# Kernel tuning notes

Measured on AMD Instinct MI355X. Metric: run time of the kernel, lower is better.

The kernel has to match this reference:

```python
import jax, jax.numpy as jnp
import numpy as np

N_EMBD = 1024
HEAD_SIZE = 64
WINDOW_SIZE = 256


def setup_inputs() -> dict:
    key = jax.random.key(0)
    kx, kk, kq, kv = jax.random.split(key, 4)
    B, T = 4, 4096
    x = jax.random.normal(kx, (B, T, N_EMBD), dtype=jnp.float32)
    # Linear(n_embd, head_size, bias=False): y = x @ W where W is [n_embd, head_size]
    scale = 1.0 / np.sqrt(N_EMBD)
    Wk = jax.random.normal(kk, (N_EMBD, HEAD_SIZE), dtype=jnp.float32) * scale
    Wq = jax.random.normal(kq, (N_EMBD, HEAD_SIZE), dtype=jnp.float32) * scale
    Wv = jax.random.normal(kv, (N_EMBD, HEAD_SIZE), dtype=jnp.float32) * scale
    return {"x": x, "Wk": Wk, "Wq": Wq, "Wv": Wv}


def reference(x, Wk, Wq, Wv):
    B, T, C = x.shape
    k = jnp.einsum('btc,ch->bth', x, Wk)  # [B,T,H]
    q = jnp.einsum('btc,ch->bth', x, Wq)
    v = jnp.einsum('btc,ch->bth', x, Wv)
    scale = k.shape[-1] ** -0.5
    weights = jnp.einsum('bqh,bkh->bqk', q, k) * scale  # [B,T,T]
    rows = jnp.arange(T)[:, None]
    cols = jnp.arange(T)[None, :]
    # causal AND within sliding window of WINDOW_SIZE
    mask = (rows >= cols) & (cols >= rows - WINDOW_SIZE + 1)
    weights = jnp.where(mask, weights, -jnp.inf)
    weights = jax.nn.softmax(weights, axis=-1)
    out = jnp.einsum('bqk,bkh->bqh', weights, v)  # [B,T,H]
    return out
```

## Files before the change

kernel.cpp:

```cpp
#include <hip/hip_runtime.h>
#include <float.h>

#define TSEQ 4096
#define CEMB 1024
#define NH 64
#define WIN 256

typedef __attribute__((ext_vector_type(8))) short  s16x8;
typedef __attribute__((ext_vector_type(4))) short  s16x4;
typedef __attribute__((ext_vector_type(4))) float  f32x4;

__device__ __forceinline__ void split2(float f, short& hi, short& lo) {
    unsigned b = __float_as_uint(f);
    hi = (short)(b >> 16);
    float hf = __uint_as_float(b & 0xFFFF0000u);
    lo = (short)(__float_as_uint(f - hf) >> 16);
}

__device__ __forceinline__ void split8(f32x4 a, f32x4 b, s16x8& hi, s16x8& lo) {
    #pragma unroll
    for (int j = 0; j < 4; ++j) { short h, l; split2(a[j], h, l); hi[j] = h; lo[j] = l; }
    #pragma unroll
    for (int j = 0; j < 4; ++j) { short h, l; split2(b[j], h, l); hi[4+j] = h; lo[4+j] = l; }
}

#define MFMA(a, b, c) __builtin_amdgcn_mfma_f32_16x16x32_bf16((a), (b), (c), 0, 0, 0)

__global__ __launch_bounds__(256)
void w_convert(const float* __restrict__ Wk, const float* __restrict__ Wq,
               const float* __restrict__ Wv,
               short* __restrict__ Wth, short* __restrict__ Wtl)
{
    const int m  = blockIdx.x >> 4;
    const int k0 = (blockIdx.x & 15) << 6;
    const float* src = (m == 0) ? Wk : ((m == 1) ? Wq : Wv);
    #pragma unroll
    for (int i = 0; i < 16; ++i) {
        const int idx = threadIdx.x + (i << 8);
        const int r = idx >> 6, c = idx & 63;
        const float v = src[(k0 + r) * NH + c];
        short h, l; split2(v, h, l);
        const int o = (m * 64 + c) * CEMB + k0 + r;
        Wth[o] = h; Wtl[o] = l;
    }
}

__device__ __forceinline__ int swz(int row, int chunk) {
    return row * 32 + (((chunk) ^ ((row >> 1) & 3)) << 3);
}

__global__ __launch_bounds__(256)
void qkv_proj(const float* __restrict__ x,
              const short* __restrict__ Wth, const short* __restrict__ Wtl,
              float* __restrict__ kb, float* __restrict__ qb, float* __restrict__ vb)
{
    __shared__ short Ah[2][64 * 32], Al[2][64 * 32];
    __shared__ short Bh[2][192 * 32], Bl[2][192 * 32];

    const int tid = threadIdx.x;
    const int m0  = blockIdx.x << 6;
    const int w   = tid >> 6;
    const int l15 = tid & 15;
    const int g   = (tid >> 4) & 3;

    const int arow = tid >> 2;
    const int ach  = tid & 3;
    const float* xp = x + (size_t)(m0 + arow) * CEMB + (ach << 3);

    int wn[3], wch[3];
    #pragma unroll
    for (int i = 0; i < 3; ++i) {
        const int c = tid + (i << 8);
        wn[i] = c >> 2; wch[i] = c & 3;
    }

    f32x4 acc[4][3];
    #pragma unroll
    for (int i = 0; i < 4; ++i)
        #pragma unroll
        for (int j = 0; j < 3; ++j) acc[i][j] = (f32x4){0.f, 0.f, 0.f, 0.f};

    f32x4 xr0 = *(const f32x4*)(xp);
    f32x4 xr1 = *(const f32x4*)(xp + 4);
    s16x8 wrh[3], wrl[3];
    #pragma unroll
    for (int i = 0; i < 3; ++i) {
        const int o = wn[i] * CEMB + (wch[i] << 3);
        wrh[i] = *(const s16x8*)&Wth[o];
        wrl[i] = *(const s16x8*)&Wtl[o];
    }

    for (int t = 0; t < 32; ++t) {
        const int cur = t & 1;
        {
            s16x8 vh, vl; split8(xr0, xr1, vh, vl);
            const int ao = swz(arow, ach);
            *(s16x8*)&Ah[cur][ao] = vh;
            *(s16x8*)&Al[cur][ao] = vl;
            #pragma unroll
            for (int i = 0; i < 3; ++i) {
                const int bo = swz(wn[i], wch[i]);
                *(s16x8*)&Bh[cur][bo] = wrh[i];
                *(s16x8*)&Bl[cur][bo] = wrl[i];
            }
        }
        __syncthreads();
        if (t < 31) {
            const int k0 = (t + 1) << 5;
            xr0 = *(const f32x4*)(xp + k0);
            xr1 = *(const f32x4*)(xp + k0 + 4);
            #pragma unroll
            for (int i = 0; i < 3; ++i) {
                const int o = wn[i] * CEMB + k0 + (wch[i] << 3);
                wrh[i] = *(const s16x8*)&Wth[o];
                wrl[i] = *(const s16x8*)&Wtl[o];
            }
        }
        s16x8 afh[4], afl[4], bfh[3], bfl[3];
        #pragma unroll
        for (int rt = 0; rt < 4; ++rt) {
            const int o = swz(rt * 16 + l15, g);
            afh[rt] = *(const s16x8*)&Ah[cur][o];
            afl[rt] = *(const s16x8*)&Al[cur][o];
        }
        #pragma unroll
        for (int ct = 0; ct < 3; ++ct) {
            const int n = w * 48 + ct * 16 + l15;
            const int o = swz(n, g);
            bfh[ct] = *(const s16x8*)&Bh[cur][o];
            bfl[ct] = *(const s16x8*)&Bl[cur][o];
        }
        #pragma unroll
        for (int rt = 0; rt < 4; ++rt)
            #pragma unroll
            for (int ct = 0; ct < 3; ++ct) {
                acc[rt][ct] = MFMA(afh[rt], bfh[ct], acc[rt][ct]);
                acc[rt][ct] = MFMA(afh[rt], bfl[ct], acc[rt][ct]);
                acc[rt][ct] = MFMA(afl[rt], bfh[ct], acc[rt][ct]);
            }
    }

    #pragma unroll
    for (int ct = 0; ct < 3; ++ct) {
        const int colbase = w * 48 + ct * 16;
        float* op = (colbase < 64) ? kb : ((colbase < 128) ? qb : vb);
        const int col = (colbase & 63) + l15;
        #pragma unroll
        for (int rt = 0; rt < 4; ++rt)
            #pragma unroll
            for (int r = 0; r < 4; ++r) {
                const int row = m0 + rt * 16 + g * 4 + r;
                op[(size_t)row * NH + col] = acc[rt][ct][r];
            }
    }
}

__global__ __launch_bounds__(256)
void attn_swin(const float* __restrict__ qb, const float* __restrict__ kb,
               const float* __restrict__ vb, float* __restrict__ out)
{
    __shared__ short Kh[64 * 72], Kl[64 * 72];
    __shared__ short Vth[64 * 72], Vtl[64 * 72];
    __shared__ short Ph[4][16 * 72], Pl[4][16 * 72];

    const int tid = threadIdx.x;
    const int Q0  = blockIdx.x << 6;
    const size_t base = (size_t)blockIdx.y * TSEQ;
    const int w   = tid >> 6;
    const int l15 = tid & 15;
    const int g   = (tid >> 4) & 3;

    const int qrow = Q0 + w * 16 + l15;

    s16x8 Qh[2], Ql[2];
    #pragma unroll
    for (int ks = 0; ks < 2; ++ks) {
        const float* qp = qb + (base + qrow) * NH + ks * 32 + g * 8;
        f32x4 a = *(const f32x4*)qp;
        f32x4 b = *(const f32x4*)(qp + 4);
        split8(a, b, Qh[ks], Ql[ks]);
    }

    f32x4 O[4];
    #pragma unroll
    for (int i = 0; i < 4; ++i) O[i] = (f32x4){0.f, 0.f, 0.f, 0.f};
    float m_run = -FLT_MAX, l_run = 0.f;

    int lo = Q0 - (WIN - 1); if (lo < 0) lo = 0;
    const int t_lo = lo >> 6, t_hi = Q0 >> 6;

    for (int t = t_lo; t <= t_hi; ++t) {
        const int k0 = t << 6;
        __syncthreads();
        #pragma unroll
        for (int i = 0; i < 4; ++i) {
            const int idx = tid + (i << 8);
            const int key = idx >> 4, c4 = (idx & 15) << 2;
            f32x4 kv = *(const f32x4*)&kb[(base + k0 + key) * NH + c4];
            s16x4 h, l;
            #pragma unroll
            for (int j = 0; j < 4; ++j) { short hh, ll; split2(kv[j], hh, ll); h[j] = hh; l[j] = ll; }
            *(s16x4*)&Kh[key * 72 + c4] = h;
            *(s16x4*)&Kl[key * 72 + c4] = l;
        }
        #pragma unroll
        for (int i = 0; i < 2; ++i) {
            const int item = tid + (i << 8);
            const int dim = item & 63, kb8 = (item >> 6) << 3;
            f32x4 v0, v1;
            #pragma unroll
            for (int kk = 0; kk < 4; ++kk)
                v0[kk] = vb[(base + k0 + kb8 + kk) * NH + dim];
            #pragma unroll
            for (int kk = 0; kk < 4; ++kk)
                v1[kk] = vb[(base + k0 + kb8 + 4 + kk) * NH + dim];
            s16x8 h, l; split8(v0, v1, h, l);
            *(s16x8*)&Vth[dim * 72 + kb8] = h;
            *(s16x8*)&Vtl[dim * 72 + kb8] = l;
        }
        __syncthreads();

        f32x4 S[4];
        #pragma unroll
        for (int kt = 0; kt < 4; ++kt) {
            f32x4 s = (f32x4){0.f, 0.f, 0.f, 0.f};
            #pragma unroll
            for (int ks = 0; ks < 2; ++ks) {
                const int o = (kt * 16 + l15) * 72 + ks * 32 + g * 8;
                s16x8 kah = *(const s16x8*)&Kh[o];
                s16x8 kal = *(const s16x8*)&Kl[o];
                s = MFMA(kah, Qh[ks], s);
                s = MFMA(kah, Ql[ks], s);
                s = MFMA(kal, Qh[ks], s);
            }
            S[kt] = s;
        }

        float sv[16]; bool vd[16];
        float mt = -FLT_MAX;
        #pragma unroll
        for (int kt = 0; kt < 4; ++kt)
            #pragma unroll
            for (int r = 0; r < 4; ++r) {
                const int key = k0 + kt * 16 + g * 4 + r;
                const float s = S[kt][r] * 0.125f;
                const bool v = (key <= qrow) && (key > qrow - WIN);
                sv[kt * 4 + r] = s; vd[kt * 4 + r] = v;
                if (v) mt = fmaxf(mt, s);
            }
        mt = fmaxf(mt, __shfl_xor(mt, 16));
        mt = fmaxf(mt, __shfl_xor(mt, 32));
        const float mn  = fmaxf(m_run, mt);
        const float fsc = __expf(m_run - mn);
        float sum = 0.f;
        #pragma unroll
        for (int kt = 0; kt < 4; ++kt)
            #pragma unroll
            for (int r = 0; r < 4; ++r) {
                const float p = vd[kt * 4 + r] ? __expf(sv[kt * 4 + r] - mn) : 0.f;
                sum += p;
                short h, l; split2(p, h, l);
                const int pc = kt * 16 + g * 4 + r;
                Ph[w][l15 * 72 + pc] = h;
                Pl[w][l15 * 72 + pc] = l;
            }
        sum += __shfl_xor(sum, 16);
        sum += __shfl_xor(sum, 32);
        l_run = l_run * fsc + sum;
        m_run = mn;

        float fr[4];
        #pragma unroll
        for (int r = 0; r < 4; ++r) fr[r] = __shfl(fsc, g * 4 + r);
        #pragma unroll
        for (int dt = 0; dt < 4; ++dt)
            #pragma unroll
            for (int r = 0; r < 4; ++r) O[dt][r] *= fr[r];

        #pragma unroll
        for (int ks = 0; ks < 2; ++ks) {
            const int po = l15 * 72 + ks * 32 + g * 8;
            s16x8 pah = *(const s16x8*)&Ph[w][po];
            s16x8 pal = *(const s16x8*)&Pl[w][po];
            #pragma unroll
            for (int dt = 0; dt < 4; ++dt) {
                const int vo = (dt * 16 + l15) * 72 + ks * 32 + g * 8;
                s16x8 vbh = *(const s16x8*)&Vth[vo];
                s16x8 vbl = *(const s16x8*)&Vtl[vo];
                O[dt] = MFMA(pah, vbh, O[dt]);
                O[dt] = MFMA(pah, vbl, O[dt]);
                O[dt] = MFMA(pal, vbh, O[dt]);
            }
        }
    }

    const float linv = 1.f / l_run;
    float fr[4];
    #pragma unroll
    for (int r = 0; r < 4; ++r) fr[r] = __shfl(linv, g * 4 + r);
    #pragma unroll
    for (int dt = 0; dt < 4; ++dt)
        #pragma unroll
        for (int r = 0; r < 4; ++r) {
            const int row = Q0 + w * 16 + g * 4 + r;
            out[(base + row) * NH + dt * 16 + l15] = O[dt][r] * fr[r];
        }
}

extern "C" void kernel_launch(void* const* d_in, const int* in_sizes, int n_in,
                              void* d_out, int out_size, void* d_ws, size_t ws_size,
                              hipStream_t stream)
{
    const float* x  = (const float*)d_in[0];
    const float* Wk = (const float*)d_in[1];
    const float* Wq = (const float*)d_in[2];
    const float* Wv = (const float*)d_in[3];
    float* out = (float*)d_out;

    const int Bn = in_sizes[0] / (TSEQ * CEMB);
    const size_t perBuf = (size_t)Bn * TSEQ * NH;

    float* kb = (float*)d_ws;
    float* qb = kb + perBuf;
    float* vb = qb + perBuf;
    short* Wth = (short*)(vb + perBuf);
    short* Wtl = Wth + 192 * CEMB;

    w_convert<<<dim3(48), dim3(256), 0, stream>>>(Wk, Wq, Wv, Wth, Wtl);
    qkv_proj<<<dim3((Bn * TSEQ) / 64), dim3(256), 0, stream>>>(x, Wth, Wtl, kb, qb, vb);
    attn_swin<<<dim3(TSEQ / 64, Bn), dim3(256), 0, stream>>>(qb, kb, vb, out);
}
```

Before: 153.5 us.

## Store QKV as bf16 hi/lo pairs, pre-transpose V, split-K attention across warps

The projection kernel now writes Q/K/V already split into bf16 high/low halves and uses 32-row tiles to launch twice as many blocks. A new kernel pre-transposes V so the attention kernel can read K and V fragments straight from global memory without staging them in shared memory or synchronising per tile. Attention now gives each block 16 query rows and spreads the key tiles across its four warps, then merges the partial softmax states through shared memory. This aims to remove the repeated fp32-to-bf16 conversion and the per-tile barriers, and to raise parallelism. In exchange it adds an extra kernel launch and more workspace traffic, and K/V are now read uncached from global memory by several blocks that share the same keys.

```diff
diff --git a/kernel.cpp b/kernel.cpp
--- a/kernel.cpp
+++ b/kernel.cpp
@@ -7,21 +7,21 @@
 #define WIN 256
 
 typedef __attribute__((ext_vector_type(8))) short  s16x8;
-typedef __attribute__((ext_vector_type(4))) short  s16x4;
 typedef __attribute__((ext_vector_type(4))) float  f32x4;
-
-__device__ __forceinline__ void split2(float f, short& hi, short& lo) {
+typedef unsigned short ush;
+
+__device__ __forceinline__ void split2(float f, ush& hi, ush& lo) {
     unsigned b = __float_as_uint(f);
-    hi = (short)(b >> 16);
+    hi = (ush)(b >> 16);
     float hf = __uint_as_float(b & 0xFFFF0000u);
-    lo = (short)(__float_as_uint(f - hf) >> 16);
+    lo = (ush)(__float_as_uint(f - hf) >> 16);
 }
 
 __device__ __forceinline__ void split8(f32x4 a, f32x4 b, s16x8& hi, s16x8& lo) {
     #pragma unroll
-    for (int j = 0; j < 4; ++j) { short h, l; split2(a[j], h, l); hi[j] = h; lo[j] = l; }
-    #pragma unroll
-    for (int j = 0; j < 4; ++j) { short h, l; split2(b[j], h, l); hi[4+j] = h; lo[4+j] = l; }
+    for (int j = 0; j < 4; ++j) { ush h, l; split2(a[j], h, l); hi[j] = (short)h; lo[j] = (short)l; }
+    #pragma unroll
+    for (int j = 0; j < 4; ++j) { ush h, l; split2(b[j], h, l); hi[4+j] = (short)h; lo[4+j] = (short)l; }
 }
 
 #define MFMA(a, b, c) __builtin_amdgcn_mfma_f32_16x16x32_bf16((a), (b), (c), 0, 0, 0)
@@ -29,7 +29,7 @@
 __global__ __launch_bounds__(256)
 void w_convert(const float* __restrict__ Wk, const float* __restrict__ Wq,
                const float* __restrict__ Wv,
-               short* __restrict__ Wth, short* __restrict__ Wtl)
+               ush* __restrict__ Wth, ush* __restrict__ Wtl)
 {
     const int m  = blockIdx.x >> 4;
     const int k0 = (blockIdx.x & 15) << 6;
@@ -39,7 +39,7 @@
         const int idx = threadIdx.x + (i << 8);
         const int r = idx >> 6, c = idx & 63;
         const float v = src[(k0 + r) * NH + c];
-        short h, l; split2(v, h, l);
+        ush h, l; split2(v, h, l);
         const int o = (m * 64 + c) * CEMB + k0 + r;
         Wth[o] = h; Wtl[o] = l;
     }
@@ -51,21 +51,24 @@
 
 __global__ __launch_bounds__(256)
 void qkv_proj(const float* __restrict__ x,
-              const short* __restrict__ Wth, const short* __restrict__ Wtl,
-              float* __restrict__ kb, float* __restrict__ qb, float* __restrict__ vb)
-{
-    __shared__ short Ah[2][64 * 32], Al[2][64 * 32];
+              const ush* __restrict__ Wth, const ush* __restrict__ Wtl,
+              ush* __restrict__ kbh, ush* __restrict__ kbl,
+              ush* __restrict__ qbh, ush* __restrict__ qbl,
+              ush* __restrict__ vbh, ush* __restrict__ vbl)
+{
+    __shared__ short Ah[2][32 * 32], Al[2][32 * 32];
     __shared__ short Bh[2][192 * 32], Bl[2][192 * 32];
 
     const int tid = threadIdx.x;
-    const int m0  = blockIdx.x << 6;
+    const int m0  = blockIdx.x << 5;
     const int w   = tid >> 6;
     const int l15 = tid & 15;
     const int g   = (tid >> 4) & 3;
 
-    const int arow = tid >> 2;
-    const int ach  = tid & 3;
-    const float* xp = x + (size_t)(m0 + arow) * CEMB + (ach << 3);
+    const bool aact = tid < 128;
+    const int arow  = tid >> 2;
+    const int ach   = tid & 3;
+    const float* xp = x + (size_t)(m0 + (aact ? arow : 0)) * CEMB + (ach << 3);
 
     int wn[3], wch[3];
     #pragma unroll
@@ -74,14 +77,14 @@
         wn[i] = c >> 2; wch[i] = c & 3;
     }
 
-    f32x4 acc[4][3];
-    #pragma unroll
-    for (int i = 0; i < 4; ++i)
+    f32x4 acc[2][3];
+    #pragma unroll
+    for (int i = 0; i < 2; ++i)
         #pragma unroll
         for (int j = 0; j < 3; ++j) acc[i][j] = (f32x4){0.f, 0.f, 0.f, 0.f};
 
-    f32x4 xr0 = *(const f32x4*)(xp);
-    f32x4 xr1 = *(const f32x4*)(xp + 4);
+    f32x4 xr0 = {0,0,0,0}, xr1 = {0,0,0,0};
+    if (aact) { xr0 = *(const f32x4*)(xp); xr1 = *(const f32x4*)(xp + 4); }
     s16x8 wrh[3], wrl[3];
     #pragma unroll
     for (int i = 0; i < 3; ++i) {
@@ -92,23 +95,22 @@
 
     for (int t = 0; t < 32; ++t) {
         const int cur = t & 1;
-        {
+        if (aact) {
             s16x8 vh, vl; split8(xr0, xr1, vh, vl);
             const int ao = swz(arow, ach);
             *(s16x8*)&Ah[cur][ao] = vh;
             *(s16x8*)&Al[cur][ao] = vl;
-            #pragma unroll
-            for (int i = 0; i < 3; ++i) {
-                const int bo = swz(wn[i], wch[i]);
-                *(s16x8*)&Bh[cur][bo] = wrh[i];
-                *(s16x8*)&Bl[cur][bo] = wrl[i];
-            }
+        }
+        #pragma unroll
+        for (int i = 0; i < 3; ++i) {
+            const int bo = swz(wn[i], wch[i]);
+            *(s16x8*)&Bh[cur][bo] = wrh[i];
+            *(s16x8*)&Bl[cur][bo] = wrl[i];
         }
         __syncthreads();
         if (t < 31) {
             const int k0 = (t + 1) << 5;
-            xr0 = *(const f32x4*)(xp + k0);
-            xr1 = *(const f32x4*)(xp + k0 + 4);
+            if (aact) { xr0 = *(const f32x4*)(xp + k0); xr1 = *(const f32x4*)(xp + k0 + 4); }
             #pragma unroll
             for (int i = 0; i < 3; ++i) {
                 const int o = wn[i] * CEMB + k0 + (wch[i] << 3);
@@ -116,22 +118,21 @@
                 wrl[i] = *(const s16x8*)&Wtl[o];
             }
         }
-        s16x8 afh[4], afl[4], bfh[3], bfl[3];
-        #pragma unroll
-        for (int rt = 0; rt < 4; ++rt) {
+        s16x8 afh[2], afl[2], bfh[3], bfl[3];
+        #pragma unroll
+        for (int rt = 0; rt < 2; ++rt) {
             const int o = swz(rt * 16 + l15, g);
             afh[rt] = *(const s16x8*)&Ah[cur][o];
             afl[rt] = *(const s16x8*)&Al[cur][o];
         }
         #pragma unroll
         for (int ct = 0; ct < 3; ++ct) {
-            const int n = w * 48 + ct * 16 + l15;
-            const int o = swz(n, g);
+            const int o = swz(w * 48 + ct * 16 + l15, g);
             bfh[ct] = *(const s16x8*)&Bh[cur][o];
             bfl[ct] = *(const s16x8*)&Bl[cur][o];
         }
         #pragma unroll
-        for (int rt = 0; rt < 4; ++rt)
+        for (int rt = 0; rt < 2; ++rt)
             #pragma unroll
             for (int ct = 0; ct < 3; ++ct) {
                 acc[rt][ct] = MFMA(afh[rt], bfh[ct], acc[rt][ct]);
@@ -143,42 +144,78 @@
     #pragma unroll
     for (int ct = 0; ct < 3; ++ct) {
         const int colbase = w * 48 + ct * 16;
-        float* op = (colbase < 64) ? kb : ((colbase < 128) ? qb : vb);
+        ush* oph; ush* opl;
+        if (colbase < 64)       { oph = kbh; opl = kbl; }
+        else if (colbase < 128) { oph = qbh; opl = qbl; }
+        else                    { oph = vbh; opl = vbl; }
         const int col = (colbase & 63) + l15;
         #pragma unroll
-        for (int rt = 0; rt < 4; ++rt)
+        for (int rt = 0; rt < 2; ++rt)
             #pragma unroll
             for (int r = 0; r < 4; ++r) {
-                const int row = m0 + rt * 16 + g * 4 + r;
-                op[(size_t)row * NH + col] = acc[rt][ct][r];
+                const size_t row = m0 + rt * 16 + g * 4 + r;
+                ush h, l; split2(acc[rt][ct][r], h, l);
+                oph[row * NH + col] = h;
+                opl[row * NH + col] = l;
             }
     }
 }
 
 __global__ __launch_bounds__(256)
-void attn_swin(const float* __restrict__ qb, const float* __restrict__ kb,
-               const float* __restrict__ vb, float* __restrict__ out)
-{
-    __shared__ short Kh[64 * 72], Kl[64 * 72];
-    __shared__ short Vth[64 * 72], Vtl[64 * 72];
-    __shared__ short Ph[4][16 * 72], Pl[4][16 * 72];
+void v_transpose(const ush* __restrict__ vbh, const ush* __restrict__ vbl,
+                 ush* __restrict__ vbTh, ush* __restrict__ vbTl)
+{
+    const int k0  = blockIdx.x << 6;
+    const int b   = blockIdx.y;
+    const int dim = threadIdx.x & 63;
+    const int j16 = threadIdx.x >> 6;
+    const size_t inb = ((size_t)b * TSEQ + k0 + j16 * 16) * NH + dim;
+    s16x8 h0, h1, l0, l1;
+    #pragma unroll
+    for (int j = 0; j < 8; ++j) {
+        h0[j] = (short)vbh[inb + (size_t)j * NH];
+        l0[j] = (short)vbl[inb + (size_t)j * NH];
+    }
+    #pragma unroll
+    for (int j = 0; j < 8; ++j) {
+        h1[j] = (short)vbh[inb + (size_t)(8 + j) * NH];
+        l1[j] = (short)vbl[inb + (size_t)(8 + j) * NH];
+    }
+    const size_t ob = (size_t)b * (64 * TSEQ) + (size_t)dim * TSEQ + k0 + j16 * 16;
+    *(s16x8*)&vbTh[ob]     = h0;
+    *(s16x8*)&vbTh[ob + 8] = h1;
+    *(s16x8*)&vbTl[ob]     = l0;
+    *(s16x8*)&vbTl[ob + 8] = l1;
+}
+
+__global__ __launch_bounds__(256)
+void attn_swin(const ush* __restrict__ qbh, const ush* __restrict__ qbl,
+               const ush* __restrict__ kbh, const ush* __restrict__ kbl,
+               const ush* __restrict__ vbTh, const ush* __restrict__ vbTl,
+               float* __restrict__ out)
+{
+    __shared__ ush Ph[4][16 * 64], Pl[4][16 * 64];
+    __shared__ float cO[4][16][68];
+    __shared__ float cm[4][16], cl[4][16];
 
     const int tid = threadIdx.x;
-    const int Q0  = blockIdx.x << 6;
-    const size_t base = (size_t)blockIdx.y * TSEQ;
     const int w   = tid >> 6;
     const int l15 = tid & 15;
     const int g   = (tid >> 4) & 3;
-
-    const int qrow = Q0 + w * 16 + l15;
+    const int u   = l15 & 7;
+    const int q0  = blockIdx.x << 4;
+    const int b   = blockIdx.y;
+    const size_t tbase = (size_t)b * TSEQ;
+    const size_t vtb   = (size_t)b * (64 * TSEQ);
+
+    const int qrow = q0 + l15;
 
     s16x8 Qh[2], Ql[2];
     #pragma unroll
     for (int ks = 0; ks < 2; ++ks) {
-        const float* qp = qb + (base + qrow) * NH + ks * 32 + g * 8;
-        f32x4 a = *(const f32x4*)qp;
-        f32x4 b = *(const f32x4*)(qp + 4);
-        split8(a, b, Qh[ks], Ql[ks]);
+        const size_t o = (tbase + qrow) * NH + ks * 32 + g * 8;
+        Qh[ks] = *(const s16x8*)&qbh[o];
+        Ql[ks] = *(const s16x8*)&qbl[o];
     }
 
     f32x4 O[4];
@@ -186,39 +223,11 @@
     for (int i = 0; i < 4; ++i) O[i] = (f32x4){0.f, 0.f, 0.f, 0.f};
     float m_run = -FLT_MAX, l_run = 0.f;
 
-    int lo = Q0 - (WIN - 1); if (lo < 0) lo = 0;
-    const int t_lo = lo >> 6, t_hi = Q0 >> 6;
-
-    for (int t = t_lo; t <= t_hi; ++t) {
+    int lo = q0 - (WIN - 1); if (lo < 0) lo = 0;
+    const int t_lo = lo >> 6, t_hi = q0 >> 6;
+
+    for (int t = t_lo + w; t <= t_hi; t += 4) {
         const int k0 = t << 6;
-        __syncthreads();
-        #pragma unroll
-        for (int i = 0; i < 4; ++i) {
-            const int idx = tid + (i << 8);
-            const int key = idx >> 4, c4 = (idx & 15) << 2;
-            f32x4 kv = *(const f32x4*)&kb[(base + k0 + key) * NH + c4];
-            s16x4 h, l;
-            #pragma unroll
-            for (int j = 0; j < 4; ++j) { short hh, ll; split2(kv[j], hh, ll); h[j] = hh; l[j] = ll; }
-            *(s16x4*)&Kh[key * 72 + c4] = h;
-            *(s16x4*)&Kl[key * 72 + c4] = l;
-        }
-        #pragma unroll
-        for (int i = 0; i < 2; ++i) {
-            const int item = tid + (i << 8);
-            const int dim = item & 63, kb8 = (item >> 6) << 3;
-            f32x4 v0, v1;
-            #pragma unroll
-            for (int kk = 0; kk < 4; ++kk)
-                v0[kk] = vb[(base + k0 + kb8 + kk) * NH + dim];
-            #pragma unroll
-            for (int kk = 0; kk < 4; ++kk)
-                v1[kk] = vb[(base + k0 + kb8 + 4 + kk) * NH + dim];
-            s16x8 h, l; split8(v0, v1, h, l);
-            *(s16x8*)&Vth[dim * 72 + kb8] = h;
-            *(s16x8*)&Vtl[dim * 72 + kb8] = l;
-        }
-        __syncthreads();
 
         f32x4 S[4];
         #pragma unroll
@@ -226,17 +235,16 @@
             f32x4 s = (f32x4){0.f, 0.f, 0.f, 0.f};
             #pragma unroll
             for (int ks = 0; ks < 2; ++ks) {
-                const int o = (kt * 16 + l15) * 72 + ks * 32 + g * 8;
-                s16x8 kah = *(const s16x8*)&Kh[o];
-                s16x8 kal = *(const s16x8*)&Kl[o];
-                s = MFMA(kah, Qh[ks], s);
-                s = MFMA(kah, Ql[ks], s);
-                s = MFMA(kal, Qh[ks], s);
+                const size_t o = (tbase + k0 + kt * 16 + l15) * NH + ks * 32 + g * 8;
+                s16x8 kh = *(const s16x8*)&kbh[o];
+                s16x8 kl = *(const s16x8*)&kbl[o];
+                s = MFMA(kh, Qh[ks], s);
+                s = MFMA(kh, Ql[ks], s);
+                s = MFMA(kl, Qh[ks], s);
             }
             S[kt] = s;
         }
 
-        float sv[16]; bool vd[16];
         float mt = -FLT_MAX;
         #pragma unroll
         for (int kt = 0; kt < 4; ++kt)
@@ -244,26 +252,34 @@
             for (int r = 0; r < 4; ++r) {
                 const int key = k0 + kt * 16 + g * 4 + r;
                 const float s = S[kt][r] * 0.125f;
-                const bool v = (key <= qrow) && (key > qrow - WIN);
-                sv[kt * 4 + r] = s; vd[kt * 4 + r] = v;
-                if (v) mt = fmaxf(mt, s);
+                S[kt][r] = s;
+                if ((key <= qrow) && (key > qrow - WIN)) mt = fmaxf(mt, s);
             }
         mt = fmaxf(mt, __shfl_xor(mt, 16));
         mt = fmaxf(mt, __shfl_xor(mt, 32));
         const float mn  = fmaxf(m_run, mt);
         const float fsc = __expf(m_run - mn);
+
         float sum = 0.f;
         #pragma unroll
-        for (int kt = 0; kt < 4; ++kt)
-            #pragma unroll
-            for (int r = 0; r < 4; ++r) {
-                const float p = vd[kt * 4 + r] ? __expf(sv[kt * 4 + r] - mn) : 0.f;
-                sum += p;
-                short h, l; split2(p, h, l);
-                const int pc = kt * 16 + g * 4 + r;
-                Ph[w][l15 * 72 + pc] = h;
-                Pl[w][l15 * 72 + pc] = l;
-            }
+        for (int kt = 0; kt < 4; ++kt) {
+            const int chunk = kt * 2 + (g >> 1);
+            const int c2 = (chunk + u) & 7;
+            const int abase = l15 * 64 + c2 * 8 + (g & 1) * 4;
+            #pragma unroll
+            for (int rp = 0; rp < 4; rp += 2) {
+                const int key0 = k0 + kt * 16 + g * 4 + rp;
+                const bool v0 = (key0     <= qrow) && (key0     > qrow - WIN);
+                const bool v1 = (key0 + 1 <= qrow) && (key0 + 1 > qrow - WIN);
+                const float p0 = v0 ? __expf(S[kt][rp]     - mn) : 0.f;
+                const float p1 = v1 ? __expf(S[kt][rp + 1] - mn) : 0.f;
+                sum += p0 + p1;
+                ush h0, lo0, h1, lo1;
+                split2(p0, h0, lo0); split2(p1, h1, lo1);
+                *(unsigned int*)&Ph[w][abase + rp] = (unsigned int)h0  | ((unsigned int)h1  << 16);
+                *(unsigned int*)&Pl[w][abase + rp] = (unsigned int)lo0 | ((unsigned int)lo1 << 16);
+            }
+        }
         sum += __shfl_xor(sum, 16);
         sum += __shfl_xor(sum, 32);
         l_run = l_run * fsc + sum;
@@ -279,32 +295,46 @@
 
         #pragma unroll
         for (int ks = 0; ks < 2; ++ks) {
-            const int po = l15 * 72 + ks * 32 + g * 8;
+            const int c2r = ((ks * 4 + g) + u) & 7;
+            const int po = l15 * 64 + c2r * 8;
             s16x8 pah = *(const s16x8*)&Ph[w][po];
             s16x8 pal = *(const s16x8*)&Pl[w][po];
             #pragma unroll
             for (int dt = 0; dt < 4; ++dt) {
-                const int vo = (dt * 16 + l15) * 72 + ks * 32 + g * 8;
-                s16x8 vbh = *(const s16x8*)&Vth[vo];
-                s16x8 vbl = *(const s16x8*)&Vtl[vo];
-                O[dt] = MFMA(pah, vbh, O[dt]);
-                O[dt] = MFMA(pah, vbl, O[dt]);
-                O[dt] = MFMA(pal, vbh, O[dt]);
-            }
-        }
-    }
-
-    const float linv = 1.f / l_run;
-    float fr[4];
-    #pragma unroll
-    for (int r = 0; r < 4; ++r) fr[r] = __shfl(linv, g * 4 + r);
+                const size_t vo = vtb + (size_t)(dt * 16 + l15) * TSEQ + k0 + ks * 32 + g * 8;
+                s16x8 vh = *(const s16x8*)&vbTh[vo];
+                s16x8 vl = *(const s16x8*)&vbTl[vo];
+                O[dt] = MFMA(pah, vh, O[dt]);
+                O[dt] = MFMA(pah, vl, O[dt]);
+                O[dt] = MFMA(pal, vh, O[dt]);
+            }
+        }
+    }
+
+    if (g == 0) { cm[w][l15] = m_run; cl[w][l15] = l_run; }
     #pragma unroll
     for (int dt = 0; dt < 4; ++dt)
         #pragma unroll
+        for (int r = 0; r < 4; ++r)
+            cO[w][g * 4 + r][dt * 16 + l15] = O[dt][r];
+    __syncthreads();
+
+    {
+        const int dt = w;
+        #pragma unroll
         for (int r = 0; r < 4; ++r) {
-            const int row = Q0 + w * 16 + g * 4 + r;
-            out[(base + row) * NH + dt * 16 + l15] = O[dt][r] * fr[r];
-        }
+            const int row = g * 4 + r;
+            const float mm0 = cm[0][row], mm1 = cm[1][row], mm2 = cm[2][row], mm3 = cm[3][row];
+            const float ms = fmaxf(fmaxf(mm0, mm1), fmaxf(mm2, mm3));
+            const float f0 = __expf(mm0 - ms), f1 = __expf(mm1 - ms);
+            const float f2 = __expf(mm2 - ms), f3 = __expf(mm3 - ms);
+            const float ll = f0 * cl[0][row] + f1 * cl[1][row] + f2 * cl[2][row] + f3 * cl[3][row];
+            const int col = dt * 16 + l15;
+            const float oo = f0 * cO[0][row][col] + f1 * cO[1][row][col]
+                           + f2 * cO[2][row][col] + f3 * cO[3][row][col];
+            out[(tbase + q0 + row) * NH + col] = oo / ll;
+        }
+    }
 }
 
 extern "C" void kernel_launch(void* const* d_in, const int* in_sizes, int n_in,
@@ -320,13 +350,22 @@
     const int Bn = in_sizes[0] / (TSEQ * CEMB);
     const size_t perBuf = (size_t)Bn * TSEQ * NH;
 
-    float* kb = (float*)d_ws;
-    float* qb = kb + perBuf;
-    float* vb = qb + perBuf;
-    short* Wth = (short*)(vb + perBuf);
-    short* Wtl = Wth + 192 * CEMB;
+    ush* base = (ush*)d_ws;
+    ush* kbh = base;
+    ush* kbl = kbh + perBuf;
+    ush* qbh = kbl + perBuf;
+    ush* qbl = qbh + perBuf;
+    ush* vbh = qbl + perBuf;
+    ush* vbl = vbh + perBuf;
+    ush* vbTh = vbl + perBuf;
+    ush* vbTl = vbTh + perBuf;
+    ush* Wth = vbTl + perBuf;
+    ush* Wtl = Wth + 192 * CEMB;
 
     w_convert<<<dim3(48), dim3(256), 0, stream>>>(Wk, Wq, Wv, Wth, Wtl);
-    qkv_proj<<<dim3((Bn * TSEQ) / 64), dim3(256), 0, stream>>>(x, Wth, Wtl, kb, qb, vb);
-    attn_swin<<<dim3(TSEQ / 64, Bn), dim3(256), 0, stream>>>(qb, kb, vb, out);
-}
+    qkv_proj<<<dim3((Bn * TSEQ) / 32), dim3(256), 0, stream>>>(x, Wth, Wtl,
+                                                               kbh, kbl, qbh, qbl, vbh, vbl);
+    v_transpose<<<dim3(TSEQ / 64, Bn), dim3(256), 0, stream>>>(vbh, vbl, vbTh, vbTl);
+    attn_swin<<<dim3(TSEQ / 16, Bn), dim3(256), 0, stream>>>(qbh, qbl, kbh, kbl,
+                                                             vbTh, vbTl, out);
+}
```

Measured after the change: 173.2 us. 12.8% more time.
